# Optimization experiments

Measured on AMD Instinct MI355X. Metric: run time of the kernel, lower is better.

Reference implementation:

```python
import jax, jax.numpy as jnp
import numpy as np

N = 2048
H = W = 128
TANFOVX = TANFOVY = 0.5
SCALE_MOD = 1.0
ZNEAR = 0.2
ALPHA_MIN = 1.0 / 255.0
ALPHA_MAX = 0.99


def setup_inputs() -> dict:
    key = jax.random.key(0)
    ks = jax.random.split(key, 6)
    # gaussians in a frustum-ish box in front of the camera
    base = jax.random.uniform(ks[0], (N, 3), dtype=jnp.float32)
    means3D = base * jnp.array([4.0, 4.0, 5.0]) + jnp.array([-2.0, -2.0, 3.0])
    means2D = jnp.zeros((N, 3), dtype=jnp.float32)  # screenspace grad placeholder (unused in math)
    opacities = jax.random.uniform(ks[1], (N, 1), dtype=jnp.float32) * 0.9 + 0.05
    colors_precomp = jax.random.uniform(ks[2], (N, 3), dtype=jnp.float32)
    scales = jax.random.uniform(ks[3], (N, 3), dtype=jnp.float32) * 0.08 + 0.01
    rotations = jax.random.normal(ks[4], (N, 4), dtype=jnp.float32)
    bg = jnp.zeros((3,), dtype=jnp.float32)
    viewmatrix = jnp.eye(4, dtype=jnp.float32)
    return {"means3D": means3D, "means2D": means2D, "opacities": opacities,
            "colors_precomp": colors_precomp, "scales": scales,
            "rotations": rotations, "bg": bg, "viewmatrix": viewmatrix}


def _quat_to_rotmat(q):
    # q: [N,4] (w,x,y,z), normalized
    q = q / jnp.linalg.norm(q, axis=-1, keepdims=True)
    r, x, y, z = q[:, 0], q[:, 1], q[:, 2], q[:, 3]
    R = jnp.stack([
        1 - 2 * (y * y + z * z), 2 * (x * y - r * z), 2 * (x * z + r * y),
        2 * (x * y + r * z), 1 - 2 * (x * x + z * z), 2 * (y * z - r * x),
        2 * (x * z - r * y), 2 * (y * z + r * x), 1 - 2 * (x * x + y * y),
    ], axis=-1).reshape(-1, 3, 3)
    return R


def reference(means3D, means2D, opacities, colors_precomp, scales, rotations, bg, viewmatrix):
    fx = W / (2.0 * TANFOVX)
    fy = H / (2.0 * TANFOVY)
    # ---- 3D covariance from scale/rotation ----
    R = _quat_to_rotmat(rotations)                      # [N,3,3]
    M = R * (scales * SCALE_MOD)[:, None, :]            # R @ diag(s)
    cov3D = jnp.einsum('nij,nkj->nik', M, M)            # [N,3,3]
    # ---- view transform ----
    Wm = viewmatrix[:3, :3]
    t = means3D @ Wm.T + viewmatrix[:3, 3]              # [N,3] camera space
    tz = t[:, 2]
    limx, limy = 1.3 * TANFOVX, 1.3 * TANFOVY
    txz = jnp.clip(t[:, 0] / tz, -limx, limx) * tz
    tyz = jnp.clip(t[:, 1] / tz, -limy, limy) * tz
    # ---- EWA 2x3 Jacobian ----
    zero = jnp.zeros_like(tz)
    J = jnp.stack([
        jnp.stack([fx / tz, zero, -fx * txz / (tz * tz)], axis=-1),
        jnp.stack([zero, fy / tz, -fy * tyz / (tz * tz)], axis=-1),
    ], axis=1)                                          # [N,2,3]
    T = jnp.einsum('nij,jk->nik', J, Wm)                # [N,2,3]
    cov2D = jnp.einsum('nij,njk,nlk->nil', T, cov3D, T) # [N,2,2]
    a = cov2D[:, 0, 0] + 0.3                            # low-pass dilation
    b = cov2D[:, 0, 1]
    c = cov2D[:, 1, 1] + 0.3
    det = a * c - b * b
    det_safe = jnp.where(det > 0, det, 1.0)
    conA, conB, conC = c / det_safe, -b / det_safe, a / det_safe
    # ---- projected pixel centers ----
    px = fx * t[:, 0] / tz + (W - 1) * 0.5
    py = fy * t[:, 1] / tz + (H - 1) * 0.5
    valid = (det > 0) & (tz > ZNEAR)
    # ---- global depth sort (front to back) ----
    order = jnp.argsort(tz)
    px, py = px[order], py[order]
    conA, conB, conC = conA[order], conB[order], conC[order]
    opac = opacities[order, 0]
    cols = colors_precomp[order]
    valid = valid[order]
    # ---- per-pixel evaluation ----
    ys, xs = jnp.meshgrid(jnp.arange(H, dtype=jnp.float32),
                          jnp.arange(W, dtype=jnp.float32), indexing='ij')
    xs = xs.reshape(-1)
    ys = ys.reshape(-1)
    dx = xs[:, None] - px[None, :]                      # [P,N]
    dy = ys[:, None] - py[None, :]
    power = -0.5 * (conA * dx * dx + conC * dy * dy) - conB * dx * dy
    alpha = jnp.minimum(ALPHA_MAX, opac * jnp.exp(power))
    alpha = jnp.where((power > 0) | (alpha < ALPHA_MIN) | (~valid), 0.0, alpha)
    # ---- front-to-back alpha compositing ----
    one_m = 1.0 - alpha
    cum = jnp.cumprod(one_m, axis=1)                    # [P,N]
    T_excl = jnp.pad(cum[:, :-1], ((0, 0), (1, 0)), constant_values=1.0)
    wgt = T_excl * alpha                                # [P,N]
    rgb = wgt @ cols                                    # [P,3]
    out = rgb + cum[:, -1:] * bg[None, :]               # residual transmittance * bg
    return out.reshape(H, W, 3).transpose(2, 0, 1)      # [3,H,W]
```

## Files before the change

### kernel.cpp

```cpp
#include <hip/hip_runtime.h>
#include <math.h>

#define N_G 2048
#define IMG_H 128
#define IMG_W 128

constexpr float FX = 128.0f;
constexpr float FY = 128.0f;
constexpr float LIMX = 0.65f;
constexpr float LIMY = 0.65f;
constexpr float ZNEAR_C = 0.2f;
constexpr float ALPHA_MIN_C = 1.0f / 255.0f;
constexpr float ALPHA_MAX_C = 0.99f;

struct VMc { float m[12]; };

template <bool WANT_COLOR>
__device__ __forceinline__ void compute_g(
    int i,
    const float* __restrict__ means3D, const float* __restrict__ opac_in,
    const float* __restrict__ cols, const float* __restrict__ scales,
    const float* __restrict__ rots, const VMc& vm,
    float& px, float& py, float& cA, float& cB, float& cC,
    float& op, float& cr, float& cg, float& cb, float& pcut,
    float& tzv, unsigned int& bb)
{
    float mx = means3D[3*i+0], my = means3D[3*i+1], mz = means3D[3*i+2];
    float q0 = rots[4*i+0], q1 = rots[4*i+1], q2 = rots[4*i+2], q3 = rots[4*i+3];
    float qn = 1.0f / sqrtf(q0*q0 + q1*q1 + q2*q2 + q3*q3);
    float r = q0*qn, x = q1*qn, y = q2*qn, z = q3*qn;

    float R00 = 1.0f - 2.0f*(y*y + z*z), R01 = 2.0f*(x*y - r*z), R02 = 2.0f*(x*z + r*y);
    float R10 = 2.0f*(x*y + r*z), R11 = 1.0f - 2.0f*(x*x + z*z), R12 = 2.0f*(y*z - r*x);
    float R20 = 2.0f*(x*z - r*y), R21 = 2.0f*(y*z + r*x), R22 = 1.0f - 2.0f*(x*x + y*y);

    float s0 = scales[3*i+0], s1 = scales[3*i+1], s2 = scales[3*i+2];
    float M00 = R00*s0, M01 = R01*s1, M02 = R02*s2;
    float M10 = R10*s0, M11 = R11*s1, M12 = R12*s2;
    float M20 = R20*s0, M21 = R21*s1, M22 = R22*s2;

    float C00 = M00*M00 + M01*M01 + M02*M02;
    float C01 = M00*M10 + M01*M11 + M02*M12;
    float C02 = M00*M20 + M01*M21 + M02*M22;
    float C11 = M10*M10 + M11*M11 + M12*M12;
    float C12 = M10*M20 + M11*M21 + M12*M22;
    float C22 = M20*M20 + M21*M21 + M22*M22;

    float W00 = vm.m[0], W01 = vm.m[1], W02 = vm.m[2];
    float W10 = vm.m[4], W11 = vm.m[5], W12 = vm.m[6];
    float W20 = vm.m[8], W21 = vm.m[9], W22 = vm.m[10];
    float t0 = W00*mx + W01*my + W02*mz + vm.m[3];
    float t1 = W10*mx + W11*my + W12*mz + vm.m[7];
    float t2 = W20*mx + W21*my + W22*mz + vm.m[11];

    tzv = t2;
    float invz = 1.0f / tzv;
    float txz = fminf(fmaxf(t0*invz, -LIMX), LIMX) * tzv;
    float tyz = fminf(fmaxf(t1*invz, -LIMY), LIMY) * tzv;

    float J00 = FX*invz, J02 = -FX*txz*invz*invz;
    float J11 = FY*invz, J12 = -FY*tyz*invz*invz;

    float T00 = J00*W00 + J02*W20, T01 = J00*W01 + J02*W21, T02 = J00*W02 + J02*W22;
    float T10 = J11*W10 + J12*W20, T11 = J11*W11 + J12*W21, T12 = J11*W12 + J12*W22;

    float U00 = T00*C00 + T01*C01 + T02*C02;
    float U01 = T00*C01 + T01*C11 + T02*C12;
    float U02 = T00*C02 + T01*C12 + T02*C22;
    float U10 = T10*C00 + T11*C01 + T12*C02;
    float U11 = T10*C01 + T11*C11 + T12*C12;
    float U12 = T10*C02 + T11*C12 + T12*C22;

    float a = U00*T00 + U01*T01 + U02*T02 + 0.3f;
    float b = U00*T10 + U01*T11 + U02*T12;
    float c = U10*T10 + U11*T11 + U12*T12 + 0.3f;

    float det = a*c - b*b;
    bool valid = (det > 0.0f) && (tzv > ZNEAR_C);

    if (valid) {
        float invdet = 1.0f / det;
        cA = c * invdet;
        cB = -b * invdet;
        cC = a * invdet;
        px = FX * t0 * invz + (IMG_W - 1) * 0.5f;
        py = FY * t1 * invz + (IMG_H - 1) * 0.5f;
        op = opac_in[i];
        pcut = logf(ALPHA_MIN_C / op) - 1e-4f;
        float hx = sqrtf(fmaxf(0.0f, -2.0f * pcut * a));
        float hy = sqrtf(fmaxf(0.0f, -2.0f * pcut * c));
        int ix0 = (int)floorf(px - hx), ix1 = (int)ceilf(px + hx);
        int iy0 = (int)floorf(py - hy), iy1 = (int)ceilf(py + hy);
        if (ix1 < 0 || ix0 > IMG_W-1 || iy1 < 0 || iy0 > IMG_H-1) {
            bb = 0x000000FFu;
        } else {
            unsigned int X0 = (unsigned int)max(0, ix0), X1 = (unsigned int)min(IMG_W-1, ix1);
            unsigned int Y0 = (unsigned int)max(0, iy0), Y1 = (unsigned int)min(IMG_H-1, iy1);
            bb = X0 | (X1 << 8) | (Y0 << 16) | (Y1 << 24);
        }
    } else {
        px = 0.0f; py = 0.0f; cA = 0.0f; cB = 0.0f; cC = 0.0f;
        op = 0.0f; pcut = 1e30f;
        bb = 0x000000FFu;
    }
    if (WANT_COLOR) {
        cr = cols[3*i+0]; cg = cols[3*i+1]; cb = cols[3*i+2];
    } else {
        cr = 0.0f; cg = 0.0f; cb = 0.0f;
    }
}

#define NTHREADS 512
#define NWAVES 8

__global__ __launch_bounds__(NTHREADS) void fused_kernel(
    const float* __restrict__ means3D, const float* __restrict__ opac_in,
    const float* __restrict__ cols, const float* __restrict__ scales,
    const float* __restrict__ rots, const float* __restrict__ bg,
    const float* __restrict__ vmp, float* __restrict__ out)
{
    __shared__ float s_tz[N_G];
    __shared__ unsigned int s_bb[N_G];
    __shared__ unsigned short stmp[NWAVES][256];
    __shared__ unsigned short sidx[N_G];
    __shared__ unsigned long long skey[N_G];
    __shared__ unsigned short ssort[N_G];
    __shared__ float4 srec[NTHREADS*3];
    __shared__ float4 scomb[NWAVES*64];
    __shared__ int scnt[NWAVES], soff[NWAVES+1];

    int tid = threadIdx.x;
    int wave = tid >> 6, lane = tid & 63;
    int bx = blockIdx.x & 15, by = blockIdx.x >> 4;
    int tpx0 = bx*8, tpy0 = by*8;

    VMc vm;
    #pragma unroll
    for (int k = 0; k < 12; ++k) vm.m[k] = vmp[k];

    for (int g = tid; g < N_G; g += NTHREADS) {
        float px,py,cA,cB,cC,op,cr,cg,cb,pcut,tzv; unsigned int bb;
        compute_g<false>(g, means3D, opac_in, cols, scales, rots, vm,
                         px,py,cA,cB,cC,op,cr,cg,cb,pcut,tzv,bb);
        s_tz[g] = tzv;
        s_bb[g] = bb;
    }
    __syncthreads();

    int c = 0;
    #pragma unroll
    for (int r = 0; r < N_G/NTHREADS; ++r) {
        int j = wave*(N_G/NWAVES) + r*64 + lane;
        unsigned int bb = s_bb[j];
        int x0 = bb & 0xFF, x1 = (bb >> 8) & 0xFF;
        int y0 = (bb >> 16) & 0xFF, y1 = (bb >> 24) & 0xFF;
        bool hit = (x0 <= tpx0+7) && (x1 >= tpx0) && (y0 <= tpy0+7) && (y1 >= tpy0);
        unsigned long long m = __ballot(hit);
        if (hit) stmp[wave][c + __popcll(m & ((1ull << lane) - 1ull))] = (unsigned short)j;
        c += __popcll(m);
    }
    if (lane == 0) scnt[wave] = c;
    __syncthreads();
    if (tid == 0) { soff[0] = 0; for (int w = 0; w < NWAVES; ++w) soff[w+1] = soff[w] + scnt[w]; }
    __syncthreads();
    int cnt = soff[NWAVES];
    for (int w = 0; w < NWAVES; ++w) {
        int o = soff[w], n = scnt[w];
        for (int k = tid; k < n; k += NTHREADS) sidx[o + k] = stmp[w][k];
    }
    __syncthreads();

    for (int t = tid; t < cnt; t += NTHREADS) {
        int id = sidx[t];
        skey[t] = ((unsigned long long)__float_as_uint(s_tz[id]) << 16) | (unsigned int)id;
    }
    __syncthreads();

    for (int t = wave; t < cnt; t += NWAVES) {
        unsigned long long key_t = skey[t];
        int rank = 0;
        for (int u0 = 0; u0 < cnt; u0 += 64) {
            int u = u0 + lane;
            bool p = (u < cnt) && (skey[u] < key_t);
            rank += __popcll(__ballot(p));
        }
        if (lane == 0) ssort[rank] = (unsigned short)(key_t & 0xFFFFull);
    }
    __syncthreads();

    int pxi = tpx0 + (lane & 7), pyi = tpy0 + (lane >> 3);
    float fxp = (float)pxi, fyp = (float)pyi;

    float Tg = 1.0f, Crg = 0.0f, Cgg = 0.0f, Cbg = 0.0f;

    for (int base = 0; base < cnt; base += NTHREADS) {
        int m = cnt - base; if (m > NTHREADS) m = NTHREADS;
        if (tid < m) {
            int g = ssort[base + tid];
            float px,py,cA,cB,cC,op,cr,cg,cb,pcut,tzv; unsigned int bb;
            compute_g<true>(g, means3D, opac_in, cols, scales, rots, vm,
                            px,py,cA,cB,cC,op,cr,cg,cb,pcut,tzv,bb);
            srec[tid*3+0] = make_float4(px, py, cA, cB);
            srec[tid*3+1] = make_float4(cC, op, cr, cg);
            srec[tid*3+2] = make_float4(cb, pcut, 0.0f, 0.0f);
        }
        __syncthreads();

        int L = (m + NWAVES - 1) / NWAVES;
        int g0 = wave * L, g1 = min(m, g0 + L);
        float Ts = 1.0f, Crs = 0.0f, Cgs = 0.0f, Cbs = 0.0f;
        for (int gi = g0; gi < g1; ++gi) {
            float4 d0 = srec[gi*3+0];
            float4 d1 = srec[gi*3+1];
            float4 d2 = srec[gi*3+2];
            float dx = fxp - d0.x;
            float dy = fyp - d0.y;
            float power = -0.5f*(d0.z*dx*dx + d1.x*dy*dy) - d0.w*dx*dy;
            if (!(power > 0.0f || power < d2.y)) {
                float alpha = fminf(ALPHA_MAX_C, d1.y * __expf(power));
                if (alpha >= ALPHA_MIN_C) {
                    float w = Ts * alpha;
                    Crs += w * d1.z;
                    Cgs += w * d1.w;
                    Cbs += w * d2.x;
                    Ts *= (1.0f - alpha);
                }
            }
        }
        scomb[wave*64 + lane] = make_float4(Ts, Crs, Cgs, Cbs);
        __syncthreads();

        if (wave == 0) {
            #pragma unroll
            for (int s = 0; s < NWAVES; ++s) {
                float4 v = scomb[s*64 + lane];
                Crg += Tg * v.y;
                Cgg += Tg * v.z;
                Cbg += Tg * v.w;
                Tg  *= v.x;
            }
        }
        int alive = __syncthreads_count((tid < 64) && (Tg >= 1e-4f));
        if (alive == 0) break;
    }

    if (wave == 0) {
        float bg0 = bg[0], bg1 = bg[1], bg2 = bg[2];
        int pidx = pyi * IMG_W + pxi;
        out[0*IMG_H*IMG_W + pidx] = Crg + Tg * bg0;
        out[1*IMG_H*IMG_W + pidx] = Cgg + Tg * bg1;
        out[2*IMG_H*IMG_W + pidx] = Cbg + Tg * bg2;
    }
}

extern "C" void kernel_launch(void* const* d_in, const int* in_sizes, int n_in,
                              void* d_out, int out_size, void* d_ws, size_t ws_size,
                              hipStream_t stream) {
    const float* means3D = (const float*)d_in[0];
    const float* opac    = (const float*)d_in[2];
    const float* cols    = (const float*)d_in[3];
    const float* scales  = (const float*)d_in[4];
    const float* rots    = (const float*)d_in[5];
    const float* bg      = (const float*)d_in[6];
    const float* vm      = (const float*)d_in[7];
    float* out = (float*)d_out;

    fused_kernel<<<256, NTHREADS, 0, stream>>>(means3D, opac, cols, scales, rots, bg, vm, out);
}
```

Before: 19.57 us.

## Fuse key build, overlap per-tile sort with gaussian preprocessing in one pass

Key construction is merged into the compaction loop, which removes one barrier. When a tile has at most 512 candidates, each thread now loads its gaussian's parameters and computes its own rank by scanning all keys with scalar compares. Rendering then reads records indirectly through the sorted slot index, which removes a barrier and the separate wave-per-key ballot sort. A float4 quaternion load and a fast __logf are also added; larger tiles fall back to the old path.

```diff
diff --git a/kernel.cpp b/kernel.cpp
--- a/kernel.cpp
+++ b/kernel.cpp
@@ -26,7 +26,8 @@
     float& tzv, unsigned int& bb)
 {
     float mx = means3D[3*i+0], my = means3D[3*i+1], mz = means3D[3*i+2];
-    float q0 = rots[4*i+0], q1 = rots[4*i+1], q2 = rots[4*i+2], q3 = rots[4*i+3];
+    float4 q = *(const float4*)(rots + 4*i);
+    float q0 = q.x, q1 = q.y, q2 = q.z, q3 = q.w;
     float qn = 1.0f / sqrtf(q0*q0 + q1*q1 + q2*q2 + q3*q3);
     float r = q0*qn, x = q1*qn, y = q2*qn, z = q3*qn;
 
@@ -86,7 +87,7 @@
         px = FX * t0 * invz + (IMG_W - 1) * 0.5f;
         py = FY * t1 * invz + (IMG_H - 1) * 0.5f;
         op = opac_in[i];
-        pcut = logf(ALPHA_MIN_C / op) - 1e-4f;
+        pcut = __logf(ALPHA_MIN_C / op) - 1e-4f;
         float hx = sqrtf(fmaxf(0.0f, -2.0f * pcut * a));
         float hy = sqrtf(fmaxf(0.0f, -2.0f * pcut * c));
         int ix0 = (int)floorf(px - hx), ix1 = (int)ceilf(px + hx);
@@ -123,7 +124,7 @@
     __shared__ unsigned int s_bb[N_G];
     __shared__ unsigned short stmp[NWAVES][256];
     __shared__ unsigned short sidx[N_G];
-    __shared__ unsigned long long skey[N_G];
+    __shared__ unsigned long long skey[N_G + 8];
     __shared__ unsigned short ssort[N_G];
     __shared__ float4 srec[NTHREADS*3];
     __shared__ float4 scomb[NWAVES*64];
@@ -166,53 +167,48 @@
     int cnt = soff[NWAVES];
     for (int w = 0; w < NWAVES; ++w) {
         int o = soff[w], n = scnt[w];
-        for (int k = tid; k < n; k += NTHREADS) sidx[o + k] = stmp[w][k];
-    }
-    __syncthreads();
-
-    for (int t = tid; t < cnt; t += NTHREADS) {
-        int id = sidx[t];
-        skey[t] = ((unsigned long long)__float_as_uint(s_tz[id]) << 16) | (unsigned int)id;
-    }
-    __syncthreads();
-
-    for (int t = wave; t < cnt; t += NWAVES) {
-        unsigned long long key_t = skey[t];
-        int rank = 0;
-        for (int u0 = 0; u0 < cnt; u0 += 64) {
-            int u = u0 + lane;
-            bool p = (u < cnt) && (skey[u] < key_t);
-            rank += __popcll(__ballot(p));
-        }
-        if (lane == 0) ssort[rank] = (unsigned short)(key_t & 0xFFFFull);
-    }
+        for (int k = tid; k < n; k += NTHREADS) {
+            int id = stmp[w][k];
+            sidx[o + k] = (unsigned short)id;
+            skey[o + k] = ((unsigned long long)__float_as_uint(s_tz[id]) << 16) | (unsigned int)id;
+        }
+    }
+    if (tid < 8) skey[cnt + tid] = ~0ull;
     __syncthreads();
 
     int pxi = tpx0 + (lane & 7), pyi = tpy0 + (lane >> 3);
     float fxp = (float)pxi, fyp = (float)pyi;
-
     float Tg = 1.0f, Crg = 0.0f, Cgg = 0.0f, Cbg = 0.0f;
 
-    for (int base = 0; base < cnt; base += NTHREADS) {
-        int m = cnt - base; if (m > NTHREADS) m = NTHREADS;
-        if (tid < m) {
-            int g = ssort[base + tid];
+    if (cnt <= NTHREADS) {
+        if (tid < cnt) {
+            unsigned long long key_t = skey[tid];
+            int g = (int)(key_t & 0xFFFFull);
             float px,py,cA,cB,cC,op,cr,cg,cb,pcut,tzv; unsigned int bb;
             compute_g<true>(g, means3D, opac_in, cols, scales, rots, vm,
                             px,py,cA,cB,cC,op,cr,cg,cb,pcut,tzv,bb);
             srec[tid*3+0] = make_float4(px, py, cA, cB);
             srec[tid*3+1] = make_float4(cC, op, cr, cg);
             srec[tid*3+2] = make_float4(cb, pcut, 0.0f, 0.0f);
+            int rank = 0;
+            int cp = (cnt + 7) & ~7;
+            for (int u = 0; u < cp; u += 8) {
+                #pragma unroll
+                for (int k = 0; k < 8; ++k)
+                    rank += (skey[u+k] < key_t) ? 1 : 0;
+            }
+            ssort[rank] = (unsigned short)tid;
         }
         __syncthreads();
 
-        int L = (m + NWAVES - 1) / NWAVES;
-        int g0 = wave * L, g1 = min(m, g0 + L);
+        int L = (cnt + NWAVES - 1) / NWAVES;
+        int g0 = wave * L, g1 = min(cnt, g0 + L);
         float Ts = 1.0f, Crs = 0.0f, Cgs = 0.0f, Cbs = 0.0f;
         for (int gi = g0; gi < g1; ++gi) {
-            float4 d0 = srec[gi*3+0];
-            float4 d1 = srec[gi*3+1];
-            float4 d2 = srec[gi*3+2];
+            int slot = ssort[gi];
+            float4 d0 = srec[slot*3+0];
+            float4 d1 = srec[slot*3+1];
+            float4 d2 = srec[slot*3+2];
             float dx = fxp - d0.x;
             float dy = fyp - d0.y;
             float power = -0.5f*(d0.z*dx*dx + d1.x*dy*dy) - d0.w*dx*dy;
@@ -240,8 +236,70 @@
                 Tg  *= v.x;
             }
         }
-        int alive = __syncthreads_count((tid < 64) && (Tg >= 1e-4f));
-        if (alive == 0) break;
+    } else {
+        for (int t = tid; t < cnt; t += NTHREADS) {
+            unsigned long long key_t = skey[t];
+            int rank = 0;
+            int cp = (cnt + 7) & ~7;
+            for (int u = 0; u < cp; u += 8) {
+                #pragma unroll
+                for (int k = 0; k < 8; ++k)
+                    rank += (skey[u+k] < key_t) ? 1 : 0;
+            }
+            ssort[rank] = (unsigned short)(key_t & 0xFFFFull);
+        }
+        __syncthreads();
+
+        for (int base = 0; base < cnt; base += NTHREADS) {
+            int m = cnt - base; if (m > NTHREADS) m = NTHREADS;
+            if (tid < m) {
+                int g = ssort[base + tid];
+                float px,py,cA,cB,cC,op,cr,cg,cb,pcut,tzv; unsigned int bb;
+                compute_g<true>(g, means3D, opac_in, cols, scales, rots, vm,
+                                px,py,cA,cB,cC,op,cr,cg,cb,pcut,tzv,bb);
+                srec[tid*3+0] = make_float4(px, py, cA, cB);
+                srec[tid*3+1] = make_float4(cC, op, cr, cg);
+                srec[tid*3+2] = make_float4(cb, pcut, 0.0f, 0.0f);
+            }
+            __syncthreads();
+
+            int L = (m + NWAVES - 1) / NWAVES;
+            int g0 = wave * L, g1 = min(m, g0 + L);
+            float Ts = 1.0f, Crs = 0.0f, Cgs = 0.0f, Cbs = 0.0f;
+            for (int gi = g0; gi < g1; ++gi) {
+                float4 d0 = srec[gi*3+0];
+                float4 d1 = srec[gi*3+1];
+                float4 d2 = srec[gi*3+2];
+                float dx = fxp - d0.x;
+                float dy = fyp - d0.y;
+                float power = -0.5f*(d0.z*dx*dx + d1.x*dy*dy) - d0.w*dx*dy;
+                if (!(power > 0.0f || power < d2.y)) {
+                    float alpha = fminf(ALPHA_MAX_C, d1.y * __expf(power));
+                    if (alpha >= ALPHA_MIN_C) {
+                        float w = Ts * alpha;
+                        Crs += w * d1.z;
+                        Cgs += w * d1.w;
+                        Cbs += w * d2.x;
+                        Ts *= (1.0f - alpha);
+                    }
+                }
+            }
+            scomb[wave*64 + lane] = make_float4(Ts, Crs, Cgs, Cbs);
+            __syncthreads();
+
+            if (wave == 0) {
+                #pragma unroll
+                for (int s = 0; s < NWAVES; ++s) {
+                    float4 v = scomb[s*64 + lane];
+                    Crg += Tg * v.y;
+                    Cgg += Tg * v.z;
+                    Cbg += Tg * v.w;
+                    Tg  *= v.x;
+                }
+            }
+            int alive = __syncthreads_count((tid < 64) && (Tg >= 1e-4f));
+            if (alive == 0) break;
+        }
     }
 
     if (wave == 0) {
```

Result: faster. 18.00 us (-8.0%).
